# Optimization experiments

Measured on AMD Instinct MI355X. Metric: run time of the kernel, lower is better.

Reference implementation:

```python
import jax, jax.numpy as jnp
import numpy as np

P = 5.0
A = 10.0
NUM_VARS = 1_000_000
NUM_CLAUSES = 1_000_000
E = 3_000_000  # edges per polarity


def setup_inputs() -> dict:
    key = jax.random.key(0)
    k1, k2, k3, k4, k5 = jax.random.split(key, 5)
    xv = jax.random.uniform(k1, (NUM_VARS, 1), dtype=jnp.float32)
    # clause rows: shuffled arange % NUM_CLAUSES so every clause is non-empty
    cp = jax.random.permutation(k2, jnp.arange(E, dtype=jnp.int64) % NUM_CLAUSES)
    cn = jax.random.permutation(k3, jnp.arange(E, dtype=jnp.int64) % NUM_CLAUSES)
    vp = jax.random.randint(k4, (E,), 0, NUM_VARS, dtype=jnp.int64)
    vn = jax.random.randint(k5, (E,), 0, NUM_VARS, dtype=jnp.int64)
    adj_pos = jnp.stack([cp, vp])  # [2, E]
    adj_neg = jnp.stack([cn, vn])  # [2, E]
    clause_count = jnp.ones((NUM_CLAUSES,), dtype=jnp.float32)
    return {"xv": xv, "adj_pos": adj_pos, "adj_neg": adj_neg, "clause_count": clause_count}


def reference(xv, adj_pos, adj_neg, clause_count):
    x = xv.reshape(-1)            # [V]
    xn = 1.0 - x
    # gather literal values and their exp(p*.) weights along edges
    lit = jnp.concatenate([x[adj_pos[1]], xn[adj_neg[1]]])            # [2E]
    xe = jnp.concatenate([jnp.exp(P * x)[adj_pos[1]], jnp.exp(P * xn)[adj_neg[1]]])  # [2E]
    idx = jnp.concatenate([adj_pos[0], adj_neg[0]])                   # [2E]
    numerator = jax.ops.segment_sum(lit * xe, idx, num_segments=NUM_CLAUSES)
    dominator = jax.ops.segment_sum(xe, idx, num_segments=NUM_CLAUSES)
    # push_to_side: 1/(1+exp(a*(0.5-x))) == sigmoid(a*(x-0.5))
    sm = jax.nn.sigmoid(A * (numerator / dominator - 0.5))            # [NUM_CLAUSES]
    # metric = mse_loss(sm, clause_count)
    loss = jnp.mean((sm - clause_count) ** 2)
    return loss
```

## Files before the change

### kernel.cpp

```cpp
#include <hip/hip_runtime.h>

constexpr int   NUM_CLAUSES = 1000000;
constexpr int   NUM_EDGES   = 3000000;
constexpr float Pc = 5.0f;
constexpr float Ac = 10.0f;

constexpr float FXSCALE = 64.0f;
constexpr float FXINV   = 1.0f / 64.0f;

constexpr int NB  = 250;
constexpr int CPB = 4000;

constexpr int TPB   = 512;
constexpr int RPB   = 8192;
constexpr int RPT   = RPB / TPB;
constexpr int NBLKP = (NUM_EDGES + RPB - 1) / RPB;
constexpr int NBLK  = 2 * NBLKP;
constexpr int TW    = NB + 1;

constexpr float QSCALE = 1048575.0f;
constexpr float QINV   = 1.0f / 1048575.0f;

constexpr size_t OFF_TAB = (size_t)NBLK * RPB * sizeof(unsigned);

__device__ __forceinline__ unsigned pack_fx(float num, float den) {
    unsigned lo = (unsigned)(num * FXSCALE + 0.5f);
    unsigned hi = (unsigned)(den * FXSCALE + 0.5f);
    return lo | (hi << 16);
}

__global__ __launch_bounds__(TPB)
void partition_kernel(const int*   __restrict__ adj_pos,
                      const int*   __restrict__ adj_neg,
                      const float* __restrict__ x,
                      unsigned* __restrict__ recs,
                      unsigned* __restrict__ tabT,
                      float* __restrict__ out) {
    __shared__ unsigned hist[NB];
    __shared__ unsigned lbase[TW];
    __shared__ unsigned srec[RPB];
    __shared__ unsigned wsum[TPB / 64];
    __shared__ unsigned woff[TPB / 64];

    const int  g     = (int)blockIdx.x;
    const bool neg   = (g >= NBLKP);
    const int  sblk  = neg ? g - NBLKP : g;
    const int  start = sblk * RPB;
    const int  n     = min(RPB, NUM_EDGES - start);
    const int* crow  = neg ? adj_neg : adj_pos;
    const int* vrow  = crow + NUM_EDGES;
    const int  tid   = (int)threadIdx.x;

    if (g == 0 && tid == 0) out[0] = 0.0f;

    for (int b = tid; b < NB; b += TPB) hist[b] = 0;
    __syncthreads();

    int cc_[RPT], vv_[RPT];
    if (n == RPB) {
        #pragma unroll
        for (int j = 0; j < RPT / 4; ++j) {
            int4 c4 = ((const int4*)(crow + start))[j * TPB + tid];
            int4 v4 = ((const int4*)(vrow + start))[j * TPB + tid];
            cc_[4*j] = c4.x; cc_[4*j+1] = c4.y; cc_[4*j+2] = c4.z; cc_[4*j+3] = c4.w;
            vv_[4*j] = v4.x; vv_[4*j+1] = v4.y; vv_[4*j+2] = v4.z; vv_[4*j+3] = v4.w;
        }
    } else {
        #pragma unroll
        for (int r = 0; r < RPT; ++r) {
            int pos = 4 * ((r >> 2) * TPB + tid) + (r & 3);
            cc_[r] = (pos < n) ? crow[start + pos] : -1;
            vv_[r] = (pos < n) ? vrow[start + pos] : 0;
        }
    }

    float xv[RPT];
    #pragma unroll
    for (int r = 0; r < RPT; ++r) xv[r] = x[vv_[r]];

    unsigned rec[RPT], meta[RPT];
    #pragma unroll
    for (int r = 0; r < RPT; ++r) {
        meta[r] = 0xFFFFFFFFu;
        if (cc_[r] >= 0) {
            int   c   = cc_[r];
            int   b   = c / CPB;
            float lit = neg ? (1.0f - xv[r]) : xv[r];
            unsigned q = (unsigned)(lit * QSCALE + 0.5f);
            rec[r] = (q << 12) | (unsigned)(c - b * CPB);
            unsigned rank = atomicAdd(&hist[b], 1u);
            meta[r] = ((unsigned)b << 13) | rank;
        }
    }
    __syncthreads();

    unsigned h    = (tid < NB) ? hist[tid] : 0u;
    unsigned incl = h;
    #pragma unroll
    for (int off = 1; off < 64; off <<= 1) {
        unsigned t = __shfl_up(incl, off, 64);
        if ((tid & 63) >= off) incl += t;
    }
    if ((tid & 63) == 63) wsum[tid >> 6] = incl;
    __syncthreads();
    if (tid == 0) {
        unsigned a = 0;
        #pragma unroll
        for (int w = 0; w < TPB / 64; ++w) { woff[w] = a; a += wsum[w]; }
    }
    __syncthreads();
    if (tid < NB) lbase[tid] = incl - h + woff[tid >> 6];
    if (tid == 0) lbase[NB] = (unsigned)n;
    __syncthreads();

    #pragma unroll
    for (int r = 0; r < RPT; ++r) {
        if (meta[r] != 0xFFFFFFFFu) {
            unsigned b    = meta[r] >> 13;
            unsigned rank = meta[r] & 0x1FFFu;
            srec[lbase[b] + rank] = rec[r];
        }
    }
    __syncthreads();

    uint4* gout4 = (uint4*)(recs + (size_t)g * RPB);
    for (int p4 = tid; p4 < n / 4; p4 += TPB)
        gout4[p4] = ((const uint4*)srec)[p4];
    for (int p = (n & ~3) + tid; p < n; p += TPB)
        recs[(size_t)g * RPB + p] = srec[p];
    for (int b = tid; b < TW; b += TPB)
        tabT[(size_t)b * NBLK + g] = lbase[b];
}

__global__ __launch_bounds__(1024)
void bucket_loss_kernel(const unsigned* __restrict__ recs,
                        const unsigned* __restrict__ tabT,
                        const float* __restrict__ cc,
                        float* __restrict__ out) {
    __shared__ unsigned lacc[CPB];
    __shared__ unsigned sseg[NBLK];
    __shared__ unsigned eseg[NBLK];
    const int b    = (int)blockIdx.x;
    const int lane = (int)threadIdx.x & 63;
    const int wid  = (int)threadIdx.x >> 6;

    for (int j = threadIdx.x; j < CPB; j += 1024) lacc[j] = 0;
    for (int t = threadIdx.x; t < NBLK; t += 1024) {
        sseg[t] = tabT[(size_t)b       * NBLK + t];
        eseg[t] = tabT[(size_t)(b + 1) * NBLK + t];
    }
    __syncthreads();

    for (int blk = wid; blk < NBLK; blk += 16) {
        unsigned s = sseg[blk];
        unsigned e = eseg[blk];
        const unsigned* rr = recs + (size_t)blk * RPB;
        for (unsigned k = s + (unsigned)lane; k < e; k += 64) {
            unsigned r   = rr[k];
            float    lit = (float)(r >> 12) * QINV;
            float    w   = __expf(Pc * lit);
            atomicAdd(&lacc[r & 0xFFFu], pack_fx(lit * w, w));
        }
    }
    __syncthreads();

    float v = 0.0f;
    const float* gc = cc + (size_t)b * CPB;
    for (int j = threadIdx.x; j < CPB; j += 1024) {
        unsigned a   = lacc[j];
        float    num = (float)(a & 0xffffu) * FXINV;
        float    den = (float)(a >> 16)     * FXINV;
        float    sm  = 1.0f / (1.0f + __expf(-Ac * (num / den - 0.5f)));
        float    e0  = sm - gc[j];
        v += e0 * e0;
    }
    v *= 1.0f / (float)NUM_CLAUSES;

    #pragma unroll
    for (int off = 32; off > 0; off >>= 1)
        v += __shfl_down(v, off, 64);

    __shared__ float partial[16];
    if (lane == 0) partial[wid] = v;
    __syncthreads();
    if (threadIdx.x == 0) {
        float s = 0.f;
        #pragma unroll
        for (int w = 0; w < 16; ++w) s += partial[w];
        atomicAdd(out, s);
    }
}

extern "C" void kernel_launch(void* const* d_in, const int* in_sizes, int n_in,
                              void* d_out, int out_size, void* d_ws, size_t ws_size,
                              hipStream_t stream) {
    const float* xv      = (const float*)d_in[0];
    const int*   adj_pos = (const int*)  d_in[1];
    const int*   adj_neg = (const int*)  d_in[2];
    const float* cc      = (const float*)d_in[3];

    char* ws = (char*)d_ws;
    unsigned* recs = (unsigned*)ws;
    unsigned* tabT = (unsigned*)(ws + OFF_TAB);
    float*    out  = (float*)d_out;

    partition_kernel<<<NBLK, TPB, 0, stream>>>(adj_pos, adj_neg, xv,
                                               recs, tabT, out);

    bucket_loss_kernel<<<NB, 1024, 0, stream>>>(recs, tabT, cc, out);
}
```

Baseline: 147.3 us.

## Halve partition block size, store offset table row-major, split wavefronts across segments

Partition blocks shrink to 256 threads with 4096 records each, which doubles the block count and makes each per-bucket segment about half as long. The offset table is now written row-major per partition block, so each block's write is contiguous, and the bucket kernel reads both segment bounds as one uint2 pair. In the bucket kernel each wavefront is split into four 16-lane groups, so each group handles a different short segment (about 8 records) instead of leaving most of a 64-lane wave idle. The cost is a strided table read in the bucket kernel and twice as many segments to walk.

```diff
diff --git a/kernel.cpp b/kernel.cpp
--- a/kernel.cpp
+++ b/kernel.cpp
@@ -11,8 +11,8 @@
 constexpr int NB  = 250;
 constexpr int CPB = 4000;
 
-constexpr int TPB   = 512;
-constexpr int RPB   = 8192;
+constexpr int TPB   = 256;
+constexpr int RPB   = 4096;
 constexpr int RPT   = RPB / TPB;
 constexpr int NBLKP = (NUM_EDGES + RPB - 1) / RPB;
 constexpr int NBLK  = 2 * NBLKP;
@@ -34,7 +34,7 @@
                       const int*   __restrict__ adj_neg,
                       const float* __restrict__ x,
                       unsigned* __restrict__ recs,
-                      unsigned* __restrict__ tabT,
+                      unsigned* __restrict__ tab,
                       float* __restrict__ out) {
     __shared__ unsigned hist[NB];
     __shared__ unsigned lbase[TW];
@@ -128,34 +128,36 @@
         gout4[p4] = ((const uint4*)srec)[p4];
     for (int p = (n & ~3) + tid; p < n; p += TPB)
         recs[(size_t)g * RPB + p] = srec[p];
-    for (int b = tid; b < TW; b += TPB)
-        tabT[(size_t)b * NBLK + g] = lbase[b];
+    unsigned* trow = tab + (size_t)g * TW;
+    for (int b = tid; b < TW; b += TPB) trow[b] = lbase[b];
 }
 
 __global__ __launch_bounds__(1024)
 void bucket_loss_kernel(const unsigned* __restrict__ recs,
-                        const unsigned* __restrict__ tabT,
+                        const unsigned* __restrict__ tab,
                         const float* __restrict__ cc,
                         float* __restrict__ out) {
     __shared__ unsigned lacc[CPB];
-    __shared__ unsigned sseg[NBLK];
-    __shared__ unsigned eseg[NBLK];
+    __shared__ uint2    srange[NBLK];
     const int b    = (int)blockIdx.x;
     const int lane = (int)threadIdx.x & 63;
     const int wid  = (int)threadIdx.x >> 6;
 
     for (int j = threadIdx.x; j < CPB; j += 1024) lacc[j] = 0;
     for (int t = threadIdx.x; t < NBLK; t += 1024) {
-        sseg[t] = tabT[(size_t)b       * NBLK + t];
-        eseg[t] = tabT[(size_t)(b + 1) * NBLK + t];
-    }
-    __syncthreads();
-
-    for (int blk = wid; blk < NBLK; blk += 16) {
-        unsigned s = sseg[blk];
-        unsigned e = eseg[blk];
+        const unsigned* row = tab + (size_t)t * TW + b;
+        srange[t] = make_uint2(row[0], row[1]);
+    }
+    __syncthreads();
+
+    const int sub  = lane >> 4;
+    const int slan = lane & 15;
+    for (int base = wid * 4; base < NBLK; base += 64) {
+        int blk = base + sub;
+        unsigned s = 0, e = 0;
+        if (blk < NBLK) { uint2 se = srange[blk]; s = se.x; e = se.y; }
         const unsigned* rr = recs + (size_t)blk * RPB;
-        for (unsigned k = s + (unsigned)lane; k < e; k += 64) {
+        for (unsigned k = s + (unsigned)slan; k < e; k += 16) {
             unsigned r   = rr[k];
             float    lit = (float)(r >> 12) * QINV;
             float    w   = __expf(Pc * lit);
@@ -201,11 +203,11 @@
 
     char* ws = (char*)d_ws;
     unsigned* recs = (unsigned*)ws;
-    unsigned* tabT = (unsigned*)(ws + OFF_TAB);
+    unsigned* tab  = (unsigned*)(ws + OFF_TAB);
     float*    out  = (float*)d_out;
 
     partition_kernel<<<NBLK, TPB, 0, stream>>>(adj_pos, adj_neg, xv,
-                                               recs, tabT, out);
-
-    bucket_loss_kernel<<<NB, 1024, 0, stream>>>(recs, tabT, cc, out);
-}
+                                               recs, tab, out);
+
+    bucket_loss_kernel<<<NB, 1024, 0, stream>>>(recs, tab, cc, out);
+}
```

Result: no change. 146.6 us (-0.5%).
